# Performance work log

Measured on AMD Instinct MI355X. Metric: run time of the kernel, lower is better.

Reference implementation:

```python
import jax, jax.numpy as jnp
import numpy as np

L = 16            # num_levels
F = 4             # embedding_dim
H = 524288        # hashmap_size (2**19)
MIN_RES = 16
MAX_RES = 1024
P1 = np.int32(73856093)
P2 = np.int32(19349663)


def _resolutions():
    # torch.logspace(log10(min_res), log10(max_res), L) then round -> int32
    r = np.logspace(np.log10(float(MIN_RES)), np.log10(float(MAX_RES)), L)
    return jnp.asarray(np.round(r).astype(np.int32))  # [L]


def setup_inputs() -> dict:
    key = jax.random.key(0)
    kx, kt = jax.random.split(key)
    B = 2_097_152
    x = jax.random.uniform(kx, (B,), dtype=jnp.float32)  # values in [0,1]
    # nn.init.uniform_(weight, -1e-4, 1e-4) per level; stacked as [L,H,F]
    tables = jax.random.uniform(kt, (L, H, F), minval=-1e-4, maxval=1e-4, dtype=jnp.float32)
    return {"x": x, "tables": tables}


def reference(x, tables):
    res = _resolutions()                       # [L] int32
    levels = jnp.arange(L, dtype=jnp.int32)    # [L]
    xc = jnp.clip(x, 0.0, 1.0)                 # [B]
    t = xc[None, :] * (res - 1).astype(jnp.float32)[:, None]   # [L,B]
    i0 = jnp.floor(t).astype(jnp.int32)                         # [L,B]
    i1 = jnp.minimum(i0 + 1, (res - 1)[:, None])                # clamp(max=R-1)
    w = (t - i0.astype(jnp.float32))[..., None]                 # [L,B,1]

    def hsh(i):
        # int32 wrap-around multiply matches torch x.int() * prime1
        h = (i * P1) ^ (levels[:, None] * P2)
        return jnp.mod(h, H)                                    # non-negative, like torch %

    h0 = hsh(i0)
    h1 = hsh(i1)
    l_idx = levels[:, None]                                     # [L,1]
    e0 = tables[l_idx, h0]                                      # [L,B,F]
    e1 = tables[l_idx, h1]                                      # [L,B,F]
    e = e0 * (1.0 - w) + e1 * w                                 # [L,B,F]
    B = x.shape[0]
    # concat per-level features along last dim -> [B, L*F]
    return jnp.transpose(e, (1, 0, 2)).reshape(B, L * F)
```

## Files before the change

### kernel.cpp

```cpp
#include <hip/hip_runtime.h>

#define LVL 16
#define FEAT 4
#define HSZ 524288
#define HMASK (HSZ - 1)
#define P1 73856093u
#define P2 19349663u

#define NSTAGE 3155
#define BLOCK 1024
#define GRID 512

typedef float f32x4 __attribute__((ext_vector_type(4)));

static __device__ __constant__ int kRes[LVL] = {
    16, 21, 28, 37, 49, 64, 84, 111, 147, 194, 256, 338, 446, 588, 776, 1024
};
static __device__ __constant__ int kOff[15] = {
    0, 16, 37, 65, 102, 151, 215, 299, 410, 557, 751, 1007, 1345, 1791, 2379
};

__global__ void __launch_bounds__(BLOCK)
hashgrid1d_kernel(const float* __restrict__ x,
                  const float* __restrict__ tables,
                  float* __restrict__ out,
                  int B)
{
    __shared__ f32x4 sTab[NSTAGE];

    for (int e = threadIdx.x; e < NSTAGE; e += BLOCK) {
        int l = 0;
        #pragma unroll
        for (int k = 1; k < 15; ++k) l += (e >= kOff[k]);
        const int i = e - kOff[l];
        const unsigned h = (((unsigned)i * P1) ^ ((unsigned)l * P2)) & HMASK;
        sTab[e] = *(const f32x4*)(tables + ((size_t)l * HSZ + h) * FEAT);
    }
    __syncthreads();

    const int tid    = blockIdx.x * blockDim.x + threadIdx.x;
    const int stride = GRID * BLOCK;

    const int      l     = tid & 15;
    const bool     glob  = (l == 15);
    const int      res   = kRes[l];
    const float    resm1 = (float)(res - 1);
    const int      imax  = res - 1;
    const int      soff  = glob ? 0 : kOff[l];
    const unsigned lh    = (unsigned)l * P2;
    const float*   t15   = tables + (size_t)15 * HSZ * FEAT;

    const int total = B * LVL;
    for (int idx = tid; idx < total; idx += stride) {
        const int p = idx >> 4;

        float xc = x[p];
        xc = fminf(fmaxf(xc, 0.0f), 1.0f);

        const float t  = xc * resm1;
        const float fi = floorf(t);
        const int   i0 = (int)fi;
        const int   i1 = min(i0 + 1, imax);
        const float w  = t - fi;

        f32x4 e0, e1;
        if (!glob) {
            e0 = sTab[soff + i0];
            e1 = sTab[soff + i1];
        } else {
            const unsigned h0 = (((unsigned)i0 * P1) ^ lh) & HMASK;
            const unsigned h1 = (((unsigned)i1 * P1) ^ lh) & HMASK;
            e0 = *(const f32x4*)(t15 + (size_t)h0 * FEAT);
            e1 = *(const f32x4*)(t15 + (size_t)h1 * FEAT);
        }

        const float omw = 1.0f - w;
        const f32x4 r = e0 * omw + e1 * w;

        __builtin_nontemporal_store(r, (f32x4*)(out + (size_t)idx * FEAT));
    }
}

extern "C" void kernel_launch(void* const* d_in, const int* in_sizes, int n_in,
                              void* d_out, int out_size, void* d_ws, size_t ws_size,
                              hipStream_t stream)
{
    const float* x      = (const float*)d_in[0];
    const float* tables = (const float*)d_in[1];
    float*       out    = (float*)d_out;
    const int    B      = in_sizes[0];

    hipLaunchKernelGGL(hashgrid1d_kernel, dim3(GRID), dim3(BLOCK), 0, stream,
                       x, tables, out, B);
}
```

Measured before the change: 113.8 us.

## Stage x into LDS per block and use fixed-size block tiling

Each block now owns a contiguous chunk of 4096 points, loads their x values into LDS with one vectorized load per thread, and loops a fixed 64 iterations instead of a grid-stride loop. The grid grows from 512 blocks to B*16/65536 blocks (512 for this B), and clamping uses fmed3. This aims to cut redundant global reads of x (16 threads read the same value) and loop-bound overhead. The risk is that every block still rebuilds the full 3155-entry table stage, and the code assumes B is a multiple of 4096 with no tail handling.

New measurement: 113.9 us. About the same (+0.1%).

```diff
diff --git a/kernel.cpp b/kernel.cpp
--- a/kernel.cpp
+++ b/kernel.cpp
@@ -7,9 +7,11 @@
 #define P1 73856093u
 #define P2 19349663u
 
-#define NSTAGE 3155
+#define TSTAGE 3155
+#define XSTAGE 4096
 #define BLOCK 1024
-#define GRID 512
+#define ITERS 64
+#define LDS_BYTES (TSTAGE * 16 + XSTAGE * 4)
 
 typedef float f32x4 __attribute__((ext_vector_type(4)));
 
@@ -26,9 +28,11 @@
                   float* __restrict__ out,
                   int B)
 {
-    __shared__ f32x4 sTab[NSTAGE];
+    extern __shared__ char smem[];
+    f32x4* sTab = (f32x4*)smem;
+    float* sX   = (float*)(smem + TSTAGE * 16);
 
-    for (int e = threadIdx.x; e < NSTAGE; e += BLOCK) {
+    for (int e = threadIdx.x; e < TSTAGE; e += BLOCK) {
         int l = 0;
         #pragma unroll
         for (int k = 1; k < 15; ++k) l += (e >= kOff[k]);
@@ -36,12 +40,14 @@
         const unsigned h = (((unsigned)i * P1) ^ ((unsigned)l * P2)) & HMASK;
         sTab[e] = *(const f32x4*)(tables + ((size_t)l * HSZ + h) * FEAT);
     }
+    {
+        const f32x4 v = ((const f32x4*)x)[(size_t)blockIdx.x * (XSTAGE / 4) + threadIdx.x];
+        *(f32x4*)(sX + 4 * threadIdx.x) = v;
+    }
     __syncthreads();
 
-    const int tid    = blockIdx.x * blockDim.x + threadIdx.x;
-    const int stride = GRID * BLOCK;
-
-    const int      l     = tid & 15;
+    const int t = threadIdx.x;
+    const int      l     = t & 15;
     const bool     glob  = (l == 15);
     const int      res   = kRes[l];
     const float    resm1 = (float)(res - 1);
@@ -50,18 +56,20 @@
     const unsigned lh    = (unsigned)l * P2;
     const float*   t15   = tables + (size_t)15 * HSZ * FEAT;
 
-    const int total = B * LVL;
-    for (int idx = tid; idx < total; idx += stride) {
-        const int p = idx >> 4;
+    const size_t base_item = (size_t)blockIdx.x << 16;
 
-        float xc = x[p];
-        xc = fminf(fmaxf(xc, 0.0f), 1.0f);
+    #pragma unroll 2
+    for (int k = 0; k < ITERS; ++k) {
+        const int it = (k << 10) + t;
+        const int pl = it >> 4;
 
-        const float t  = xc * resm1;
-        const float fi = floorf(t);
+        const float xc = __builtin_amdgcn_fmed3f(sX[pl], 0.0f, 1.0f);
+
+        const float tt = xc * resm1;
+        const float fi = floorf(tt);
         const int   i0 = (int)fi;
         const int   i1 = min(i0 + 1, imax);
-        const float w  = t - fi;
+        const float w  = tt - fi;
 
         f32x4 e0, e1;
         if (!glob) {
@@ -77,7 +85,7 @@
         const float omw = 1.0f - w;
         const f32x4 r = e0 * omw + e1 * w;
 
-        __builtin_nontemporal_store(r, (f32x4*)(out + (size_t)idx * FEAT));
+        __builtin_nontemporal_store(r, (f32x4*)(out + ((base_item + it) << 2)));
     }
 }
 
@@ -90,6 +98,7 @@
     float*       out    = (float*)d_out;
     const int    B      = in_sizes[0];
 
-    hipLaunchKernelGGL(hashgrid1d_kernel, dim3(GRID), dim3(BLOCK), 0, stream,
-                       x, tables, out, B);
+    const int grid = (B * LVL) / (BLOCK * ITERS);
+    hipLaunchKernelGGL(hashgrid1d_kernel, dim3(grid), dim3(BLOCK),
+                       LDS_BYTES, stream, x, tables, out, B);
 }
```
